# Optimization experiments

Hardware: AMD Instinct MI355X
Metric: run time of the kernel (lower is better)

The kernel has to match this reference:

```python
import jax, jax.numpy as jnp
import numpy as np

B, T, C = 4, 2048, 2048
N, K = 16, 4          # query heads, kv heads
G, H = N // K, C // N # group size 4, head dim 128


def _rmsnorm(x):
    # RMSNorm over the full last (flattened N*H or K*H) axis, no scale param
    var = jnp.mean(jnp.square(x.astype(jnp.float32)), axis=-1, keepdims=True)
    return (x * jax.lax.rsqrt(var + 1e-06)).astype(x.dtype)


def _sine_table(features, length, max_timescale=10000.0):
    fraction = jnp.arange(0, features, 2, dtype=jnp.float32) / features
    timescale = max_timescale ** fraction
    sinusoid = jnp.einsum('i,j->ij', jnp.arange(length).astype(jnp.float32), 1.0 / timescale,
                          precision=jax.lax.Precision.HIGHEST)
    sinusoid = jnp.concatenate([sinusoid, sinusoid], axis=-1)  # [T, H]
    return jnp.sin(sinusoid), jnp.cos(sinusoid)


def _rotate_half(x):
    x1, x2 = jnp.split(x, 2, axis=-1)
    return jnp.concatenate([-x2, x1], axis=-1)


def setup_inputs() -> dict:
    key = jax.random.key(0)
    kx, kq, kk, kv, ko = jax.random.split(key, 5)
    q_std = float(np.sqrt(2.0 / (5.0 * C)))
    o_std = 2.0 / 24 / float(np.sqrt(N * H))  # wang init, n_layers=24
    return {
        'x': jax.random.normal(kx, (B, T, C), dtype=jnp.float32),
        'Wq': jax.random.normal(kq, (C, N * H), dtype=jnp.float32) * q_std,
        'Wk': jax.random.normal(kk, (C, K * H), dtype=jnp.float32) * q_std,
        'Wv': jax.random.normal(kv, (C, K * H), dtype=jnp.float32) * q_std,
        'Wout': jax.random.normal(ko, (N * H, C), dtype=jnp.float32) * o_std,
    }


def reference(x, Wq, Wk, Wv, Wout):
    b, t, c = x.shape
    q = _rmsnorm(x @ Wq)              # [B,T,N*H]
    k = _rmsnorm(x @ Wk)              # [B,T,K*H]
    v = x @ Wv                        # [B,T,K*H]
    q = q.reshape(b, t, K, G, H)
    k = k.reshape(b, t, K, H)
    v = v.reshape(b, t, K, H)

    sin, cos = _sine_table(H, t)      # [T,H]
    qcos, qsin = cos[None, :, None, None, :], sin[None, :, None, None, :]
    kcos, ksin = cos[None, :, None, :], sin[None, :, None, :]
    q = (q * qcos + _rotate_half(q) * qsin).astype(q.dtype)
    k = (k * kcos + _rotate_half(k) * ksin).astype(k.dtype)

    scale = jax.lax.rsqrt(jnp.array(H, dtype=jnp.float32)).astype(q.dtype)
    q = q * scale
    # full (non-causal) softmax attention; GQA: each kv head serves G query groups
    logits = jnp.einsum('btkgh,bskh->bkgts', q, k)
    probs = jax.nn.softmax(logits.astype(jnp.float32), axis=-1).astype(logits.dtype)
    enc = jnp.einsum('bkgts,bskh->btkgh', probs, v)  # [B,T,K,G,H]
    return enc.reshape(b, t, N * H) @ Wout
```

## Files before the change

kernel.cpp:

```cpp
#include <hip/hip_runtime.h>
#include <hip/hip_bf16.h>
#include <math.h>

typedef __attribute__((ext_vector_type(4))) float f32x4;
typedef __attribute__((ext_vector_type(8))) short s16x8;
typedef __attribute__((ext_vector_type(4))) short s16x4;

#define BB 4
#define TT 2048
#define CC 2048
#define NHEAD 16
#define KVH 4
#define HD 128
#define BT (BB*TT)
#define NHC 2048
#define KHC 512
#define QKVC 3072

__device__ __forceinline__ float bf2f(unsigned short u) {
  union { unsigned u; float f; } v; v.u = ((unsigned)u) << 16; return v.f;
}
__device__ __forceinline__ unsigned short f2bf(float f) {
  union { float f; unsigned u; } v; v.f = f;
  unsigned r = v.u + 0x7fff + ((v.u >> 16) & 1);
  return (unsigned short)(r >> 16);
}

__device__ __forceinline__ void glld16(const void* gsrc, void* ldsbase) {
  __builtin_amdgcn_global_load_lds(
      (const __attribute__((address_space(1))) unsigned int*)gsrc,
      (__attribute__((address_space(3))) unsigned int*)(unsigned int)(unsigned long long)ldsbase,
      16, 0, 0);
}

#if defined(__has_builtin)
#if __has_builtin(__builtin_amdgcn_mfma_f32_16x16x16bf16_1k)
#define MFMA16(a, b, c) __builtin_amdgcn_mfma_f32_16x16x16bf16_1k((a), (b), (c), 0, 0, 0)
#elif __has_builtin(__builtin_amdgcn_mfma_f32_16x16x16_bf16)
#define MFMA16(a, b, c) __builtin_amdgcn_mfma_f32_16x16x16_bf16((a), (b), (c), 0, 0, 0)
#endif
#endif
#ifndef MFMA16
__device__ __forceinline__ f32x4 mfma16_asm(s16x4 a, s16x4 b, f32x4 c) {
  f32x4 d;
  asm volatile("s_nop 1\n\tv_mfma_f32_16x16x16_bf16 %0, %1, %2, %3"
               : "=v"(d) : "v"(a), "v"(b), "v"(c));
  return d;
}
#define MFMA16(a, b, c) mfma16_asm((a), (b), (c))
#define MFMA16_ASM_FALLBACK 1
#endif

__global__ void cvt_f2b(const float* __restrict__ in, unsigned short* __restrict__ out, int n4) {
  int i = blockIdx.x * 256 + threadIdx.x;
  if (i >= n4) return;
  float4 v = ((const float4*)in)[i];
  ushort4 o;
  o.x = f2bf(v.x); o.y = f2bf(v.y); o.z = f2bf(v.z); o.w = f2bf(v.w);
  ((ushort4*)out)[i] = o;
}

__global__ void trans_f2b(const float* __restrict__ in, unsigned short* __restrict__ out, int R, int Cc) {
  __shared__ float tile[32][33];
  int c0 = blockIdx.x * 32, r0 = blockIdx.y * 32;
  int tx = threadIdx.x, ty = threadIdx.y;
  #pragma unroll
  for (int k = 0; k < 4; k++)
    tile[ty + 8*k][tx] = in[(size_t)(r0 + ty + 8*k) * Cc + c0 + tx];
  __syncthreads();
  #pragma unroll
  for (int k = 0; k < 4; k++)
    out[(size_t)(c0 + ty + 8*k) * R + r0 + tx] = f2bf(tile[tx][ty + 8*k]);
}

__global__ void trans_v(const unsigned short* __restrict__ qkv, unsigned short* __restrict__ vT) {
  __shared__ unsigned short tile[32][33];
  int slice = blockIdx.z;
  int s0 = blockIdx.x * 32, h0 = blockIdx.y * 32;
  int tx = threadIdx.x, ty = threadIdx.y;
  const unsigned short* in = qkv + (size_t)(slice >> 2) * TT * QKVC + (NHC + KHC) + (slice & 3) * HD;
  unsigned short* out = vT + (size_t)slice * HD * TT;
  #pragma unroll
  for (int k = 0; k < 4; k++)
    tile[ty + 8*k][tx] = in[(size_t)(s0 + ty + 8*k) * QKVC + h0 + tx];
  __syncthreads();
  #pragma unroll
  for (int k = 0; k < 4; k++)
    out[(size_t)(h0 + ty + 8*k) * TT + s0 + tx] = tile[tx][ty + 8*k];
}

__global__ void sincos_init(float* __restrict__ stab, float* __restrict__ ctab) {
  int idx = blockIdx.x * 256 + threadIdx.x;
  if (idx >= TT * 64) return;
  int t = idx >> 6, i = idx & 63;
  double inv = exp(-log(10000.0) * ((double)i / 64.0));
  double ang = (double)t * inv;
  stab[idx] = (float)sin(ang);
  ctab[idx] = (float)cos(ang);
}

template<int OUTBF16>
__global__ __launch_bounds__(256) void gemm_nt(
    const unsigned short* __restrict__ A, const unsigned short* __restrict__ Bt,
    void* __restrict__ outp, int M, int Nn, int Kd) {
  __shared__ unsigned short As[128 * 32];
  __shared__ unsigned short Bs[128 * 32];
  int tid = threadIdx.x;
  int wave = tid >> 6, lane = tid & 63, q4 = lane >> 4, l16 = lane & 15;
  int m0 = blockIdx.y * 128, n0 = blockIdx.x * 128;
  int wm = (wave & 1) * 64, wn = (wave >> 1) * 64;
  f32x4 acc[4][4];
  #pragma unroll
  for (int i = 0; i < 4; i++)
    #pragma unroll
    for (int j = 0; j < 4; j++) acc[i][j] = f32x4{0.f, 0.f, 0.f, 0.f};

  int r0s = wave * 32 + (lane >> 2);
  int r1s = r0s + 16;
  int cg0 = (lane & 3) ^ ((r0s >> 1) & 3);
  int cg1 = (lane & 3) ^ ((r1s >> 1) & 3);
  const unsigned short* Ag0 = A + (size_t)(m0 + r0s) * Kd + cg0 * 8;
  const unsigned short* Ag1 = A + (size_t)(m0 + r1s) * Kd + cg1 * 8;
  const unsigned short* Bg0 = Bt + (size_t)(n0 + r0s) * Kd + cg0 * 8;
  const unsigned short* Bg1 = Bt + (size_t)(n0 + r1s) * Kd + cg1 * 8;
  unsigned short* lA0 = As + (wave * 2 + 0) * 512;
  unsigned short* lA1 = As + (wave * 2 + 1) * 512;
  unsigned short* lB0 = Bs + (wave * 2 + 0) * 512;
  unsigned short* lB1 = Bs + (wave * 2 + 1) * 512;

  int aoff[4], boff[4];
  #pragma unroll
  for (int f = 0; f < 4; f++) {
    int Ra = wm + f * 16 + l16;
    int Rb = wn + f * 16 + l16;
    aoff[f] = Ra * 32 + (q4 ^ ((Ra >> 1) & 3)) * 8;
    boff[f] = Rb * 32 + (q4 ^ ((Rb >> 1) & 3)) * 8;
  }

  for (int k0 = 0; k0 < Kd; k0 += 32) {
    __syncthreads();
    glld16(Ag0 + k0, lA0);
    glld16(Ag1 + k0, lA1);
    glld16(Bg0 + k0, lB0);
    glld16(Bg1 + k0, lB1);
    asm volatile("s_waitcnt vmcnt(0)" ::: "memory");
    __syncthreads();
    s16x8 af[4], bfr[4];
    #pragma unroll
    for (int mf = 0; mf < 4; mf++) af[mf] = *(const s16x8*)&As[aoff[mf]];
    #pragma unroll
    for (int nf = 0; nf < 4; nf++) bfr[nf] = *(const s16x8*)&Bs[boff[nf]];
    #pragma unroll
    for (int mf = 0; mf < 4; mf++)
      #pragma unroll
      for (int nf = 0; nf < 4; nf++)
        acc[mf][nf] = __builtin_amdgcn_mfma_f32_16x16x32_bf16(af[mf], bfr[nf], acc[mf][nf], 0, 0, 0);
  }
  #pragma unroll
  for (int mf = 0; mf < 4; mf++)
    #pragma unroll
    for (int nf = 0; nf < 4; nf++)
      #pragma unroll
      for (int r = 0; r < 4; r++) {
        int row = m0 + wm + mf*16 + q4*4 + r;
        int col = n0 + wn + nf*16 + l16;
        float v = acc[mf][nf][r];
        if (OUTBF16) ((unsigned short*)outp)[(size_t)row * Nn + col] = f2bf(v);
        else         ((float*)outp)[(size_t)row * Nn + col] = v;
      }
}

__global__ __launch_bounds__(256) void postproc(
    const unsigned short* __restrict__ qkv, unsigned short* __restrict__ qr,
    unsigned short* __restrict__ kr, const float* __restrict__ stab, const float* __restrict__ ctab) {
  __shared__ float sh[NHC + KHC];
  __shared__ float redq[4], redk[4];
  int row = blockIdx.x;
  int t = row & (TT - 1);
  int tid = threadIdx.x;
  const unsigned short* base = qkv + (size_t)row * QKVC;
  float sq = 0.f, sk = 0.f;
  uint4 qv = *(const uint4*)&base[tid * 8];
  const unsigned short* qp = (const unsigned short*)&qv;
  #pragma unroll
  for (int i = 0; i < 8; i++) { float f = bf2f(qp[i]); sh[tid*8 + i] = f; sq += f*f; }
  unsigned kv = *(const unsigned*)&base[NHC + tid*2];
  {
    float f0 = bf2f((unsigned short)(kv & 0xffff));
    float f1 = bf2f((unsigned short)(kv >> 16));
    sh[NHC + tid*2] = f0; sh[NHC + tid*2 + 1] = f1;
    sk += f0*f0 + f1*f1;
  }
  #pragma unroll
  for (int off = 32; off > 0; off >>= 1) { sq += __shfl_xor(sq, off); sk += __shfl_xor(sk, off); }
  if ((tid & 63) == 0) { redq[tid >> 6] = sq; redk[tid >> 6] = sk; }
  __syncthreads();
  float fq = rsqrtf((redq[0]+redq[1]+redq[2]+redq[3]) * (1.f/NHC) + 1e-6f) * 0.08838834764831845f;
  float fk = rsqrtf((redk[0]+redk[1]+redk[2]+redk[3]) * (1.f/KHC) + 1e-6f);
  #pragma unroll
  for (int pi = 0; pi < 4; pi++) {
    int P = pi * 256 + tid;
    int head = P >> 6, i = P & 63;
    float s = stab[t*64 + i], c = ctab[t*64 + i];
    float x1 = sh[head*128 + i], x2 = sh[head*128 + i + 64];
    qr[(size_t)row * NHC + head*128 + i]      = f2bf((x1*c - x2*s) * fq);
    qr[(size_t)row * NHC + head*128 + i + 64] = f2bf((x2*c + x1*s) * fq);
  }
  {
    int head = tid >> 6, i = tid & 63;
    float s = stab[t*64 + i], c = ctab[t*64 + i];
    float x1 = sh[NHC + head*128 + i], x2 = sh[NHC + head*128 + i + 64];
    kr[(size_t)row * KHC + head*128 + i]      = f2bf((x1*c - x2*s) * fk);
    kr[(size_t)row * KHC + head*128 + i + 64] = f2bf((x2*c + x1*s) * fk);
  }
}

__global__ __launch_bounds__(256, 2) void attn(
    const unsigned short* __restrict__ qr, const unsigned short* __restrict__ kr,
    const unsigned short* __restrict__ vT, unsigned short* __restrict__ enc) {
  __shared__ unsigned short Ks[128 * 128];
  __shared__ unsigned short Vs[128 * 128];
  int tid = threadIdx.x;
  int wave = tid >> 6, lane = tid & 63, q4 = lane >> 4, l16 = lane & 15;
  int bid = blockIdx.x;
  int qt = bid & 15, n = (bid >> 4) & 15, b = bid >> 8, kh = n >> 2;

  {
    size_t qbase = ((size_t)(b * TT + qt * 128)) * NHC + n * HD;
    #pragma unroll
    for (int c2 = 0; c2 < 8; c2++) {
      int flat = c2 * 256 + tid;
      int r = flat >> 4, c = flat & 15;
      *(uint4*)&Ks[r * 128 + ((c ^ (r & 7)) << 3)] =
          *(const uint4*)&qr[qbase + (size_t)r * NHC + (c << 3)];
    }
  }
  __syncthreads();
  s16x8 qf[2][4];
  #pragma unroll
  for (int qb = 0; qb < 2; qb++)
    #pragma unroll
    for (int ku = 0; ku < 4; ku++) {
      int r = wave * 32 + qb * 16 + l16;
      qf[qb][ku] = *(const s16x8*)&Ks[r * 128 + (((ku * 4 + q4) ^ (r & 7)) << 3)];
    }

  float m_st[2] = {-1e30f, -1e30f}, l_st[2] = {0.f, 0.f};
  f32x4 O[2][8];
  #pragma unroll
  for (int qb = 0; qb < 2; qb++)
    #pragma unroll
    for (int hb = 0; hb < 8; hb++) O[qb][hb] = f32x4{0.f, 0.f, 0.f, 0.f};

  for (int j = 0; j < 16; j++) {
    __syncthreads();
    {
      size_t kbase = ((size_t)(b * TT + j * 128)) * KHC + kh * HD;
      size_t vbase = ((size_t)((b * KVH + kh) * HD)) * TT + j * 128;
      #pragma unroll
      for (int c2 = 0; c2 < 8; c2++) {
        int flat = c2 * 256 + tid;
        int r = flat >> 4, c = flat & 15;
        int sw = (c ^ (r & 7)) << 3;
        *(uint4*)&Ks[r * 128 + sw] = *(const uint4*)&kr[kbase + (size_t)r * KHC + (c << 3)];
        *(uint4*)&Vs[r * 128 + sw] = *(const uint4*)&vT[vbase + (size_t)r * TT + (c << 3)];
      }
    }
    __syncthreads();
    f32x4 S[2][8];
    #pragma unroll
    for (int qb = 0; qb < 2; qb++)
      #pragma unroll
      for (int mb = 0; mb < 8; mb++) S[qb][mb] = f32x4{0.f, 0.f, 0.f, 0.f};
    #pragma unroll
    for (int mb = 0; mb < 8; mb++) {
      int r = mb * 16 + l16;
      #pragma unroll
      for (int ku = 0; ku < 4; ku++) {
        s16x8 kf = *(const s16x8*)&Ks[r * 128 + (((ku * 4 + q4) ^ (r & 7)) << 3)];
        S[0][mb] = __builtin_amdgcn_mfma_f32_16x16x32_bf16(kf, qf[0][ku], S[0][mb], 0, 0, 0);
        S[1][mb] = __builtin_amdgcn_mfma_f32_16x16x32_bf16(kf, qf[1][ku], S[1][mb], 0, 0, 0);
      }
    }
    s16x4 pf[2][8];
    #pragma unroll
    for (int qb = 0; qb < 2; qb++) {
      float mx = -1e30f;
      #pragma unroll
      for (int mb = 0; mb < 8; mb++)
        #pragma unroll
        for (int r = 0; r < 4; r++) mx = fmaxf(mx, S[qb][mb][r]);
      mx = fmaxf(mx, __shfl_xor(mx, 16));
      mx = fmaxf(mx, __shfl_xor(mx, 32));
      float mn = fmaxf(m_st[qb], mx);
      float alpha = __expf(m_st[qb] - mn);
      m_st[qb] = mn;
      float rs = 0.f;
      #pragma unroll
      for (int mb = 0; mb < 8; mb++)
        #pragma unroll
        for (int r = 0; r < 4; r++) {
          float p = __expf(S[qb][mb][r] - mn);
          rs += p;
          pf[qb][mb][r] = (short)f2bf(p);
        }
      rs += __shfl_xor(rs, 16);
      rs += __shfl_xor(rs, 32);
      l_st[qb] = l_st[qb] * alpha + rs;
      #pragma unroll
      for (int hb = 0; hb < 8; hb++) O[qb][hb] *= alpha;
    }
    #pragma unroll
    for (int su = 0; su < 8; su++) {
      #pragma unroll
      for (int hb = 0; hb < 8; hb++) {
        int r = hb * 16 + l16;
        int col4 = su * 4 + q4;
        s16x4 vf = *(const s16x4*)&Vs[r * 128 + (((col4 >> 1) ^ (r & 7)) << 3) + ((col4 & 1) << 2)];
        O[0][hb] = MFMA16(vf, pf[0][su], O[0][hb]);
        O[1][hb] = MFMA16(vf, pf[1][su], O[1][hb]);
      }
    }
  }
#ifdef MFMA16_ASM_FALLBACK
  asm volatile("s_nop 7\n\ts_nop 7\n\ts_nop 7" ::: "memory");
#endif
  #pragma unroll
  for (int qb = 0; qb < 2; qb++) {
    float inv = 1.f / l_st[qb];
    int t = b * TT + qt * 128 + wave * 32 + qb * 16 + l16;
    #pragma unroll
    for (int hb = 0; hb < 8; hb++) {
      ushort4 o;
      o.x = f2bf(O[qb][hb][0] * inv);
      o.y = f2bf(O[qb][hb][1] * inv);
      o.z = f2bf(O[qb][hb][2] * inv);
      o.w = f2bf(O[qb][hb][3] * inv);
      *(ushort4*)&enc[(size_t)t * NHC + n * HD + hb * 16 + q4 * 4] = o;
    }
  }
}

extern "C" void kernel_launch(void* const* d_in, const int* in_sizes, int n_in,
                              void* d_out, int out_size, void* d_ws, size_t ws_size,
                              hipStream_t stream) {
  const float* x  = (const float*)d_in[0];
  const float* Wq = (const float*)d_in[1];
  const float* Wk = (const float*)d_in[2];
  const float* Wv = (const float*)d_in[3];
  const float* Wo = (const float*)d_in[4];
  float* out = (float*)d_out;

  char* ws = (char*)d_ws;
  size_t off = 0;
  auto alloc = [&](size_t bytes) -> void* {
    void* p = ws + off;
    off += (bytes + 255) & ~(size_t)255;
    return p;
  };
  unsigned short* xb    = (unsigned short*)alloc((size_t)BT * CC * 2);
  unsigned short* wqkvt = (unsigned short*)alloc((size_t)QKVC * CC * 2);
  unsigned short* wot   = (unsigned short*)alloc((size_t)CC * NHC * 2);
  unsigned short* qkv   = (unsigned short*)alloc((size_t)BT * QKVC * 2);
  unsigned short* qrb   = (unsigned short*)alloc((size_t)BT * NHC * 2);
  unsigned short* krb   = (unsigned short*)alloc((size_t)BT * KHC * 2);
  unsigned short* vTb   = (unsigned short*)alloc((size_t)BB * KVH * HD * TT * 2);
  unsigned short* encb  = (unsigned short*)alloc((size_t)BT * NHC * 2);
  float* stab = (float*)alloc((size_t)TT * 64 * 4);
  float* ctab = (float*)alloc((size_t)TT * 64 * 4);

  dim3 tb(32, 8);
  cvt_f2b<<<(BT*CC/4 + 255)/256, 256, 0, stream>>>(x, xb, BT*CC/4);
  trans_f2b<<<dim3(NHC/32, CC/32), tb, 0, stream>>>(Wq, wqkvt, CC, NHC);
  trans_f2b<<<dim3(KHC/32, CC/32), tb, 0, stream>>>(Wk, wqkvt + (size_t)NHC*CC, CC, KHC);
  trans_f2b<<<dim3(KHC/32, CC/32), tb, 0, stream>>>(Wv, wqkvt + (size_t)(NHC+KHC)*CC, CC, KHC);
  trans_f2b<<<dim3(NHC/32, NHC/32), tb, 0, stream>>>(Wo, wot, NHC, CC);
  sincos_init<<<(TT*64 + 255)/256, 256, 0, stream>>>(stab, ctab);
  gemm_nt<1><<<dim3(QKVC/128, BT/128), 256, 0, stream>>>(xb, wqkvt, qkv, BT, QKVC, CC);
  postproc<<<BT, 256, 0, stream>>>(qkv, qrb, krb, stab, ctab);
  trans_v<<<dim3(TT/32, HD/32, BB*KVH), tb, 0, stream>>>(qkv, vTb);
  attn<<<BB * NHEAD * (TT/128), 256, 0, stream>>>(qrb, krb, vTb, encb);
  gemm_nt<0><<<dim3(CC/128, BT/128), 256, 0, stream>>>(encb, wot, out, BT, CC, NHC);
}
```

Before: 618.8 us.

## Prefetch K/V tiles into registers, use 16x16x32 MFMA for PV, exp2 softmax

The attention kernel now loads the next K/V tile from global memory into registers while the current tile is being computed, which hides global-load latency behind the MFMA work. The PV product switches from 16x16x16 to 16x16x32 bf16 MFMA by pairing two 4-element V fragments, halving the instruction count. Softmax uses exp2 with log2(e) folded into the Q scaling, and setprio is raised around the MFMA loops. The register prefetch raises VGPR pressure and may reduce occupancy.

```diff
diff --git a/kernel.cpp b/kernel.cpp
--- a/kernel.cpp
+++ b/kernel.cpp
@@ -26,30 +26,21 @@
   return (unsigned short)(r >> 16);
 }
 
+#if defined(__has_builtin)
+#if __has_builtin(__builtin_amdgcn_exp2f)
+#define EXP2F(x) __builtin_amdgcn_exp2f(x)
+#endif
+#endif
+#ifndef EXP2F
+#define EXP2F(x) exp2f(x)
+#endif
+
 __device__ __forceinline__ void glld16(const void* gsrc, void* ldsbase) {
   __builtin_amdgcn_global_load_lds(
       (const __attribute__((address_space(1))) unsigned int*)gsrc,
       (__attribute__((address_space(3))) unsigned int*)(unsigned int)(unsigned long long)ldsbase,
       16, 0, 0);
 }
-
-#if defined(__has_builtin)
-#if __has_builtin(__builtin_amdgcn_mfma_f32_16x16x16bf16_1k)
-#define MFMA16(a, b, c) __builtin_amdgcn_mfma_f32_16x16x16bf16_1k((a), (b), (c), 0, 0, 0)
-#elif __has_builtin(__builtin_amdgcn_mfma_f32_16x16x16_bf16)
-#define MFMA16(a, b, c) __builtin_amdgcn_mfma_f32_16x16x16_bf16((a), (b), (c), 0, 0, 0)
-#endif
-#endif
-#ifndef MFMA16
-__device__ __forceinline__ f32x4 mfma16_asm(s16x4 a, s16x4 b, f32x4 c) {
-  f32x4 d;
-  asm volatile("s_nop 1\n\tv_mfma_f32_16x16x16_bf16 %0, %1, %2, %3"
-               : "=v"(d) : "v"(a), "v"(b), "v"(c));
-  return d;
-}
-#define MFMA16(a, b, c) mfma16_asm((a), (b), (c))
-#define MFMA16_ASM_FALLBACK 1
-#endif
 
 __global__ void cvt_f2b(const float* __restrict__ in, unsigned short* __restrict__ out, int n4) {
   int i = blockIdx.x * 256 + threadIdx.x;
@@ -195,7 +186,8 @@
   for (int off = 32; off > 0; off >>= 1) { sq += __shfl_xor(sq, off); sk += __shfl_xor(sk, off); }
   if ((tid & 63) == 0) { redq[tid >> 6] = sq; redk[tid >> 6] = sk; }
   __syncthreads();
-  float fq = rsqrtf((redq[0]+redq[1]+redq[2]+redq[3]) * (1.f/NHC) + 1e-6f) * 0.08838834764831845f;
+  float fq = rsqrtf((redq[0]+redq[1]+redq[2]+redq[3]) * (1.f/NHC) + 1e-6f)
+             * (0.08838834764831845f * 1.4426950408889634f);
   float fk = rsqrtf((redk[0]+redk[1]+redk[2]+redk[3]) * (1.f/KHC) + 1e-6f);
   #pragma unroll
   for (int pi = 0; pi < 4; pi++) {
@@ -225,15 +217,24 @@
   int bid = blockIdx.x;
   int qt = bid & 15, n = (bid >> 4) & 15, b = bid >> 8, kh = n >> 2;
 
+  int tr = tid >> 4, tc = tid & 15;
+  int sw = (tc ^ (tr & 7)) << 3;
+  const unsigned short* kp0 = kr + ((size_t)(b * TT)) * KHC + kh * HD + (size_t)tr * KHC + tc * 8;
+  const unsigned short* vp0 = vT + ((size_t)((b * KVH + kh) * HD)) * TT + (size_t)tr * TT + tc * 8;
+
+  uint4 kreg[8], vreg[8];
+  #pragma unroll
+  for (int c2 = 0; c2 < 8; c2++) {
+    kreg[c2] = *(const uint4*)&kp0[(size_t)c2 * 16 * KHC];
+    vreg[c2] = *(const uint4*)&vp0[(size_t)c2 * 16 * TT];
+  }
+
   {
-    size_t qbase = ((size_t)(b * TT + qt * 128)) * NHC + n * HD;
-    #pragma unroll
-    for (int c2 = 0; c2 < 8; c2++) {
-      int flat = c2 * 256 + tid;
-      int r = flat >> 4, c = flat & 15;
-      *(uint4*)&Ks[r * 128 + ((c ^ (r & 7)) << 3)] =
-          *(const uint4*)&qr[qbase + (size_t)r * NHC + (c << 3)];
-    }
+    const unsigned short* qp = qr + ((size_t)(b * TT + qt * 128)) * NHC + n * HD
+                               + (size_t)tr * NHC + tc * 8;
+    #pragma unroll
+    for (int c2 = 0; c2 < 8; c2++)
+      *(uint4*)&Ks[(c2 * 16 + tr) * 128 + sw] = *(const uint4*)&qp[(size_t)c2 * 16 * NHC];
   }
   __syncthreads();
   s16x8 qf[2][4];
@@ -254,24 +255,27 @@
 
   for (int j = 0; j < 16; j++) {
     __syncthreads();
-    {
-      size_t kbase = ((size_t)(b * TT + j * 128)) * KHC + kh * HD;
-      size_t vbase = ((size_t)((b * KVH + kh) * HD)) * TT + j * 128;
+    #pragma unroll
+    for (int c2 = 0; c2 < 8; c2++) {
+      *(uint4*)&Ks[(c2 * 16 + tr) * 128 + sw] = kreg[c2];
+      *(uint4*)&Vs[(c2 * 16 + tr) * 128 + sw] = vreg[c2];
+    }
+    __syncthreads();
+    if (j < 15) {
+      const unsigned short* kp = kp0 + (size_t)(j + 1) * 128 * KHC;
+      const unsigned short* vp = vp0 + (size_t)(j + 1) * 128;
       #pragma unroll
       for (int c2 = 0; c2 < 8; c2++) {
-        int flat = c2 * 256 + tid;
-        int r = flat >> 4, c = flat & 15;
-        int sw = (c ^ (r & 7)) << 3;
-        *(uint4*)&Ks[r * 128 + sw] = *(const uint4*)&kr[kbase + (size_t)r * KHC + (c << 3)];
-        *(uint4*)&Vs[r * 128 + sw] = *(const uint4*)&vT[vbase + (size_t)r * TT + (c << 3)];
+        kreg[c2] = *(const uint4*)&kp[(size_t)c2 * 16 * KHC];
+        vreg[c2] = *(const uint4*)&vp[(size_t)c2 * 16 * TT];
       }
     }
-    __syncthreads();
     f32x4 S[2][8];
     #pragma unroll
     for (int qb = 0; qb < 2; qb++)
       #pragma unroll
       for (int mb = 0; mb < 8; mb++) S[qb][mb] = f32x4{0.f, 0.f, 0.f, 0.f};
+    __builtin_amdgcn_s_setprio(1);
     #pragma unroll
     for (int mb = 0; mb < 8; mb++) {
       int r = mb * 16 + l16;
@@ -282,7 +286,8 @@
         S[1][mb] = __builtin_amdgcn_mfma_f32_16x16x32_bf16(kf, qf[1][ku], S[1][mb], 0, 0, 0);
       }
     }
-    s16x4 pf[2][8];
+    __builtin_amdgcn_s_setprio(0);
+    s16x8 pf8[2][4];
     #pragma unroll
     for (int qb = 0; qb < 2; qb++) {
       float mx = -1e30f;
@@ -293,16 +298,16 @@
       mx = fmaxf(mx, __shfl_xor(mx, 16));
       mx = fmaxf(mx, __shfl_xor(mx, 32));
       float mn = fmaxf(m_st[qb], mx);
-      float alpha = __expf(m_st[qb] - mn);
+      float alpha = EXP2F(m_st[qb] - mn);
       m_st[qb] = mn;
       float rs = 0.f;
       #pragma unroll
       for (int mb = 0; mb < 8; mb++)
         #pragma unroll
         for (int r = 0; r < 4; r++) {
-          float p = __expf(S[qb][mb][r] - mn);
+          float p = EXP2F(S[qb][mb][r] - mn);
           rs += p;
-          pf[qb][mb][r] = (short)f2bf(p);
+          pf8[qb][mb >> 1][(mb & 1) * 4 + r] = (short)f2bf(p);
         }
       rs += __shfl_xor(rs, 16);
       rs += __shfl_xor(rs, 32);
@@ -310,21 +315,23 @@
       #pragma unroll
       for (int hb = 0; hb < 8; hb++) O[qb][hb] *= alpha;
     }
-    #pragma unroll
-    for (int su = 0; su < 8; su++) {
+    __builtin_amdgcn_s_setprio(1);
+    #pragma unroll
+    for (int su = 0; su < 4; su++) {
       #pragma unroll
       for (int hb = 0; hb < 8; hb++) {
         int r = hb * 16 + l16;
-        int col4 = su * 4 + q4;
-        s16x4 vf = *(const s16x4*)&Vs[r * 128 + (((col4 >> 1) ^ (r & 7)) << 3) + ((col4 & 1) << 2)];
-        O[0][hb] = MFMA16(vf, pf[0][su], O[0][hb]);
-        O[1][hb] = MFMA16(vf, pf[1][su], O[1][hb]);
+        int c0 = su * 8 + q4;
+        int c1 = c0 + 4;
+        s16x4 v0 = *(const s16x4*)&Vs[r * 128 + (((c0 >> 1) ^ (r & 7)) << 3) + ((c0 & 1) << 2)];
+        s16x4 v1 = *(const s16x4*)&Vs[r * 128 + (((c1 >> 1) ^ (r & 7)) << 3) + ((c1 & 1) << 2)];
+        s16x8 vf = __builtin_shufflevector(v0, v1, 0, 1, 2, 3, 4, 5, 6, 7);
+        O[0][hb] = __builtin_amdgcn_mfma_f32_16x16x32_bf16(vf, pf8[0][su], O[0][hb], 0, 0, 0);
+        O[1][hb] = __builtin_amdgcn_mfma_f32_16x16x32_bf16(vf, pf8[1][su], O[1][hb], 0, 0, 0);
       }
     }
-  }
-#ifdef MFMA16_ASM_FALLBACK
-  asm volatile("s_nop 7\n\ts_nop 7\n\ts_nop 7" ::: "memory");
-#endif
+    __builtin_amdgcn_s_setprio(0);
+  }
   #pragma unroll
   for (int qb = 0; qb < 2; qb++) {
     float inv = 1.f / l_st[qb];
```

Result: slower. 821.8 us (+32.8%).
